# Kernel tuning notes

Measured on AMD Instinct MI355X. Metric: run time of the kernel, lower is better.

## Reference

```python
import jax, jax.numpy as jnp
import numpy as np

LAYER_BS = 63
N_SITES = 12
B = 2048


def _kaiming_uniform(key, shape, fan_in):
    # torch kaiming_uniform_ with a=0: bound = sqrt(6/fan_in)
    bound = np.sqrt(6.0 / fan_in)
    return jax.random.uniform(key, shape, jnp.float32, -bound, bound)


def _cnn12(x, w):
    # x: (B, L, 12, Cin); w: (L, 3*Cin, Cout)
    nn0 = jnp.roll(x, -1, axis=-2) + jnp.roll(x, 3, axis=-2)
    nnn0 = jnp.roll(x, -2, axis=-2) + jnp.roll(x, 4, axis=-2)
    c0 = jnp.concatenate([nn0, nnn0], axis=-1)          # (B,L,12,2*Cin)
    c1 = c0 + jnp.roll(c0, -2, axis=-2)
    allc = jnp.concatenate([x, c1], axis=-1)            # (B,L,12,3*Cin)
    return jnp.einsum('blsc,lco->blso', allc, w)


def _batch_linear(x, w, b):
    # x: (B, L, F); w: (L, F, O); b: (L, O)
    return jnp.einsum('blf,lfo->blo', x, w) + b


def setup_inputs() -> dict:
    key = jax.random.key(0)
    ks = jax.random.split(key, 9)
    zs = jax.random.normal(ks[0], (B, LAYER_BS, N_SITES, 2), jnp.float32)
    # CNN weights: (L, 3*Cin, Cout); kaiming fan_in = 3*Cin
    w1 = _kaiming_uniform(ks[1], (LAYER_BS, 6, 32), 6)
    w2 = _kaiming_uniform(ks[2], (LAYER_BS, 96, 64), 96)
    fw1 = _kaiming_uniform(ks[3], (LAYER_BS, 128, 64), 128)
    fb1 = jax.random.uniform(ks[4], (LAYER_BS, 64), jnp.float32, -1 / np.sqrt(128), 1 / np.sqrt(128))
    fw2 = _kaiming_uniform(ks[5], (LAYER_BS, 64, 64), 64)
    fb2 = jax.random.uniform(ks[6], (LAYER_BS, 64), jnp.float32, -1 / np.sqrt(64), 1 / np.sqrt(64))
    fw3 = _kaiming_uniform(ks[7], (LAYER_BS, 64, 1), 64)
    fb3 = jax.random.uniform(ks[8], (LAYER_BS, 1), jnp.float32, -1 / np.sqrt(64), 1 / np.sqrt(64))
    return {"zs": zs, "w1": w1, "w2": w2, "fw1": fw1, "fb1": fb1,
            "fw2": fw2, "fb2": fb2, "fw3": fw3, "fb3": fb3}


def reference(zs, w1, w2, fw1, fb1, fw2, fb2, fw3, fb3):
    h = jax.nn.relu(_cnn12(zs, w1))                     # (B,L,12,32)
    h = jax.nn.relu(_cnn12(h, w2))                      # (B,L,12,64)
    h = jnp.concatenate([h.mean(axis=-2), h.max(axis=-2)], axis=-1)
    h = jax.nn.relu(_batch_linear(h, fw1, fb1))
    h = jax.nn.relu(_batch_linear(h, fw2, fb2))
    out = _batch_linear(h, fw3, fb3)                    # (B,L,1)
    return out[..., 0]                                  # (B,L)
```

## Files before the change

kernel.cpp:

```cpp
#include <hip/hip_runtime.h>


#define LNUM 63
#define BT 16
#define NBT 128
#define WSL 29184

typedef __attribute__((ext_vector_type(8))) _Float16 half8;
typedef __attribute__((ext_vector_type(2))) _Float16 half2v;
typedef __attribute__((ext_vector_type(4))) float floatx4;
typedef __attribute__((ext_vector_type(4))) unsigned uint4v;

static __device__ __forceinline__ unsigned cvtpk(float a, float b) {
    return __builtin_bit_cast(unsigned, __builtin_amdgcn_cvt_pkrtz(a, b));
}
static __device__ __forceinline__ half2v u2h(unsigned u) { return __builtin_bit_cast(half2v, u); }
static __device__ __forceinline__ float hlo16(unsigned short s) {
    return (float)__builtin_bit_cast(_Float16, s);
}
static __device__ __forceinline__ int w12(int v) { return v >= 12 ? v - 12 : v; }

#define O_POOLDW 3072
#define O_POOLUS 6144
#define O_POOL2  0
#define O_G2     1280

__global__ void prep(const float* __restrict__ w2, const float* __restrict__ fw1,
                     const float* __restrict__ fw2, const float* __restrict__ w1,
                     unsigned short* __restrict__ ws) {
    __shared__ float S[8192];
    const int l = blockIdx.x, r = blockIdx.y, t = threadIdx.x;
    if (r == 0) {
        const float4* src = (const float4*)(w2 + (size_t)l * 6144);
        #pragma unroll
        for (int j = 0; j < 6; ++j) *(float4*)(S + 4 * (t + 256 * j)) = src[t + 256 * j];
        __syncthreads();
        unsigned* dst = (unsigned*)(ws + (size_t)l * WSL);
        #pragma unroll
        for (int j = 0; j < 13; ++j) {
            int i = j * 256 + t, o = i / 52, cp = i - 52 * o, c = 2 * cp;
            dst[i] = cvtpk(S[c * 64 + o], S[c * 64 + 64 + o]);
        }
    } else if (r == 1) {
        const float4* src = (const float4*)(fw1 + (size_t)l * 8192);
        #pragma unroll
        for (int j = 0; j < 8; ++j) *(float4*)(S + 4 * (t + 256 * j)) = src[t + 256 * j];
        __syncthreads();
        unsigned* dst = (unsigned*)(ws + (size_t)l * WSL + 6656);
        #pragma unroll
        for (int j = 0; j < 17; ++j) {
            int i = j * 256 + t, o = i / 68, cp = i - 68 * o;
            dst[i] = cvtpk(S[cp * 64 + o], S[(64 + cp) * 64 + o]);
        }
    } else if (r == 2) {
        const float4* src = (const float4*)(fw2 + (size_t)l * 4096);
        #pragma unroll
        for (int j = 0; j < 4; ++j) *(float4*)(S + 4 * (t + 256 * j)) = src[t + 256 * j];
        __syncthreads();
        unsigned* dst = (unsigned*)(ws + (size_t)l * WSL + 15360);
        #pragma unroll
        for (int j = 0; j < 9; ++j) {
            int i = j * 256 + t, o = i / 36, cp = i - 36 * o, c = 2 * cp;
            dst[i] = cvtpk(S[c * 64 + o], S[c * 64 + 64 + o]);
        }
    } else {
        if (t < 192) S[t] = w1[(size_t)l * 192 + t];
        __syncthreads();
        unsigned* dst = (unsigned*)(ws + (size_t)l * WSL + 19968);
        #pragma unroll
        for (int j = 0; j < 18; ++j) {
            int i = j * 256 + t;
            int row = i / 12, kp = i - 12 * row;
            int s = row >> 5, o = row & 31;
            int d = kp - s; if (d < 0) d += 12;
            unsigned v = 0;
            if (d == 0)                                    v = cvtpk(S[o],       S[32 + o]);
            else if (d == 1 || d == 3 || d == 9 || d == 11) v = cvtpk(S[64 + o],  S[96 + o]);
            else if (d == 2 || d == 4 || d == 8 || d == 10) v = cvtpk(S[128 + o], S[160 + o]);
            dst[i] = v;
        }
    }
}

__global__ __launch_bounds__(256, 4) void fused_nn(
    const float* __restrict__ zs,  const float* __restrict__ w1,
    const float* __restrict__ fb1, const float* __restrict__ fb2,
    const float* __restrict__ fw3, const float* __restrict__ fb3,
    const unsigned short* __restrict__ ws,
    float* __restrict__ out)
{
    __shared__ __align__(16) unsigned U[4160];
    unsigned short* USH = (unsigned short*)U;

    const int t    = threadIdx.x;
    const int lane = t & 63;
    const int wv   = t >> 6;
    const int n    = lane & 15;
    const int quad = lane >> 4;
    const int l    = blockIdx.x / NBT;
    const int b0   = (blockIdx.x % NBT) * BT;

    float4 x0 = {0.f, 0.f, 0.f, 0.f}, x1 = {0.f, 0.f, 0.f, 0.f};
    if (quad < 3) {
        const float* xr = zs + ((size_t)(b0 + n) * LNUM + l) * 24 + quad * 8;
        x0 = *(const float4*)(xr);
        x1 = *(const float4*)(xr + 4);
    }
    uint4v au[6];
    {
        const uint4v* wbt = (const uint4v*)(ws + (size_t)l * WSL + 19968);
        #pragma unroll
        for (int i = 0; i < 6; ++i) {
            const int rt = 6 * wv + i;
            au[i] = (quad < 3) ? wbt[(rt * 16 + n) * 3 + quad] : (uint4v){0u, 0u, 0u, 0u};
        }
    }
    uint4v bwp[3][4];
    {
        const uint4v* w2q = (const uint4v*)(ws + (size_t)l * WSL);
        #pragma unroll
        for (int ks = 0; ks < 3; ++ks)
            #pragma unroll
            for (int nt = 0; nt < 4; ++nt)
                bwp[ks][nt] = w2q[(nt * 16 + n) * 13 + ks * 4 + quad];
    }

    half8 xb;
    {
        uint4v z = {0u, 0u, 0u, 0u};
        if (quad < 3) {
            z.x = cvtpk(x0.x, x0.y); z.y = cvtpk(x0.z, x0.w);
            z.z = cvtpk(x1.x, x1.y); z.w = cvtpk(x1.z, x1.w);
        }
        xb = __builtin_bit_cast(half8, z);
    }
    {
        #pragma unroll
        for (int i = 0; i < 6; ++i) {
            const int rt = 6 * wv + i;
            floatx4 c = __builtin_amdgcn_mfma_f32_16x16x32_f16(
                __builtin_bit_cast(half8, au[i]), xb, (floatx4){0.f, 0.f, 0.f, 0.f}, 0, 0, 0);
            unsigned pk0 = cvtpk(fmaxf(c[0], 0.f), fmaxf(c[1], 0.f));
            unsigned pk1 = cvtpk(fmaxf(c[2], 0.f), fmaxf(c[3], 0.f));
            const int s = rt >> 1;
            const int chunk = (rt & 1) * 2 + (quad >> 1);
            const int dwoff = ((chunk ^ (n & 3)) << 2) | ((quad & 1) << 1);
            *(uint2*)(U + (n * 12 + s) * 20 + dwoff) = make_uint2(pk0, pk1);
        }
    }
    const float bias1 = fb1[(size_t)l * 64 + wv * 16 + n];
    const float bias2 = fb2[(size_t)l * 64 + wv * 16 + n];
    __syncthreads();

    floatx4 acc[3][4];
    #pragma unroll
    for (int mi = 0; mi < 3; ++mi)
        #pragma unroll
        for (int nt = 0; nt < 4; ++nt) acc[mi][nt] = (floatx4){0.f, 0.f, 0.f, 0.f};
    {
        int rb_[3], si_[3], qx_[3];
        #pragma unroll
        for (int mi = 0; mi < 3; ++mi) {
            int row = 48 * wv + 16 * mi + n;
            int bi = row / 12;
            si_[mi] = row - 12 * bi;
            rb_[mi] = bi * 12;
            qx_[mi] = (quad ^ (bi & 3)) << 2;
        }
        const int dA[4] = {1, 11, 3, 9};
        const int dB[4] = {2, 10, 4, 8};
        #pragma unroll
        for (int ks = 0; ks < 3; ++ks) {
            half8 af[3];
            #pragma unroll
            for (int mi = 0; mi < 3; ++mi) {
                const int rb = rb_[mi], s = si_[mi], q4 = qx_[mi];
                if (ks == 0) {
                    af[mi] = *(const half8*)(U + (rb + s) * 20 + q4);
                } else {
                    const int* d = (ks == 1) ? dA : dB;
                    half8 l0 = *(const half8*)(U + (rb + w12(s + d[0])) * 20 + q4);
                    half8 l1 = *(const half8*)(U + (rb + w12(s + d[1])) * 20 + q4);
                    half8 l2 = *(const half8*)(U + (rb + w12(s + d[2])) * 20 + q4);
                    half8 l3 = *(const half8*)(U + (rb + w12(s + d[3])) * 20 + q4);
                    af[mi] = (l0 + l1) + (l2 + l3);
                }
            }
            #pragma unroll
            for (int mi = 0; mi < 3; ++mi)
                #pragma unroll
                for (int nt = 0; nt < 4; ++nt)
                    acc[mi][nt] = __builtin_amdgcn_mfma_f32_16x16x32_f16(
                        af[mi], __builtin_bit_cast(half8, bwp[ks][nt]), acc[mi][nt], 0, 0, 0);
        }
    }
    __syncthreads();

    #pragma unroll
    for (int mi = 0; mi < 3; ++mi) {
        const int rr = 48 * wv + 16 * mi + 4 * quad;
        const int bq = rr / 12;
        const int chk = (rr - 12 * bq) >> 2;
        #pragma unroll
        for (int nt = 0; nt < 4; ++nt) {
            const int ch = nt * 16 + n;
            float r0 = fmaxf(acc[mi][nt][0], 0.f), r1 = fmaxf(acc[mi][nt][1], 0.f);
            float r2 = fmaxf(acc[mi][nt][2], 0.f), r3 = fmaxf(acc[mi][nt][3], 0.f);
            float sm = (r0 + r1) + (r2 + r3);
            float mx = fmaxf(fmaxf(r0, r1), fmaxf(r2, r3));
            U[(bq * 64 + ch) * 3 + chk] = cvtpk(sm, mx);
        }
    }
    __builtin_amdgcn_wave_barrier();

    {
        const unsigned* p = U + t * 12;
        uint4v q0 = *(const uint4v*)(p);
        uint4v q1 = *(const uint4v*)(p + 4);
        uint4v q2 = *(const uint4v*)(p + 8);
        unsigned arr[12] = {q0.x, q0.y, q0.z, q0.w, q1.x, q1.y, q1.z, q1.w,
                            q2.x, q2.y, q2.z, q2.w};
        const int b = t >> 4, ch0 = (t * 4) & 63;
        const _Float16 inv12 = (_Float16)(1.0f / 12.0f);
        unsigned pk[4];
        #pragma unroll
        for (int j = 0; j < 4; ++j) {
            half2v d0 = u2h(arr[3 * j]), d1 = u2h(arr[3 * j + 1]), d2 = u2h(arr[3 * j + 2]);
            _Float16 s = (d0[0] + d1[0]) + d2[0];
            _Float16 m0 = d0[1] > d1[1] ? d0[1] : d1[1];
            _Float16 m  = m0 > d2[1] ? m0 : d2[1];
            half2v pm;
            pm[0] = s * inv12;
            pm[1] = m;
            pk[j] = __builtin_bit_cast(unsigned, pm);
        }
        uint2 w01 = make_uint2(pk[0], pk[1]), w23 = make_uint2(pk[2], pk[3]);
        *(uint2*)(U + O_POOLDW + b * 68 + ch0)     = w01;
        *(uint2*)(U + O_POOLDW + b * 68 + ch0 + 2) = w23;
    }
    __syncthreads();

    {
        const int o = wv * 16 + n;
        floatx4 a1 = (floatx4){bias1, bias1, bias1, bias1};
        const uint4v* f1q = (const uint4v*)(ws + (size_t)l * WSL + 6656);
        #pragma unroll
        for (int ks = 0; ks < 4; ++ks) {
            half8 av = *(const half8*)(USH + O_POOLUS + n * 136 + ks * 32 + quad * 8);
            uint4v bw = f1q[o * 17 + ks * 4 + quad];
            a1 = __builtin_amdgcn_mfma_f32_16x16x32_f16(av, __builtin_bit_cast(half8, bw), a1, 0, 0, 0);
        }
        #pragma unroll
        for (int i = 0; i < 2; ++i) {
            unsigned pk = cvtpk(fmaxf(a1[2 * i], 0.f), fmaxf(a1[2 * i + 1], 0.f));
            USH[O_POOL2 + (quad * 4 + 2 * i)     * 72 + o] = (unsigned short)(pk & 0xffffu);
            USH[O_POOL2 + (quad * 4 + 2 * i + 1) * 72 + o] = (unsigned short)(pk >> 16);
        }
    }
    __syncthreads();

    {
        const int o = wv * 16 + n;
        floatx4 a2 = (floatx4){bias2, bias2, bias2, bias2};
        const uint4v* f2q = (const uint4v*)(ws + (size_t)l * WSL + 15360);
        #pragma unroll
        for (int ks = 0; ks < 2; ++ks) {
            half8 av = *(const half8*)(USH + O_POOL2 + n * 72 + ks * 32 + quad * 8);
            uint4v bw = f2q[o * 9 + ks * 4 + quad];
            a2 = __builtin_amdgcn_mfma_f32_16x16x32_f16(av, __builtin_bit_cast(half8, bw), a2, 0, 0, 0);
        }
        #pragma unroll
        for (int i = 0; i < 2; ++i) {
            unsigned pk = cvtpk(fmaxf(a2[2 * i], 0.f), fmaxf(a2[2 * i + 1], 0.f));
            USH[O_G2 + (quad * 4 + 2 * i)     * 72 + o] = (unsigned short)(pk & 0xffffu);
            USH[O_G2 + (quad * 4 + 2 * i + 1) * 72 + o] = (unsigned short)(pk >> 16);
        }
    }
    __syncthreads();

    if (t < 16) {
        float a = fb3[l];
        const float* w3 = fw3 + (size_t)l * 64;
        #pragma unroll
        for (int c4 = 0; c4 < 16; ++c4) {
            uint2 u2 = *(const uint2*)(USH + O_G2 + t * 72 + c4 * 4);
            float4 w = *(const float4*)(w3 + c4 * 4);
            a += hlo16((unsigned short)(u2.x & 0xffff)) * w.x
               + hlo16((unsigned short)(u2.x >> 16))    * w.y
               + hlo16((unsigned short)(u2.y & 0xffff)) * w.z
               + hlo16((unsigned short)(u2.y >> 16))    * w.w;
        }
        out[(size_t)(b0 + t) * LNUM + l] = a;
    }
}

extern "C" void kernel_launch(void* const* d_in, const int* in_sizes, int n_in,
                              void* d_out, int out_size, void* d_ws, size_t ws_size,
                              hipStream_t stream) {
    const float* zs  = (const float*)d_in[0];
    const float* w1  = (const float*)d_in[1];
    const float* w2  = (const float*)d_in[2];
    const float* fw1 = (const float*)d_in[3];
    const float* fb1 = (const float*)d_in[4];
    const float* fw2 = (const float*)d_in[5];
    const float* fb2 = (const float*)d_in[6];
    const float* fw3 = (const float*)d_in[7];
    const float* fb3 = (const float*)d_in[8];
    float* out = (float*)d_out;
    unsigned short* ws = (unsigned short*)d_ws;

    hipLaunchKernelGGL(prep, dim3(LNUM, 4), dim3(256), 0, stream, w2, fw1, fw2, w1, ws);
    hipLaunchKernelGGL(fused_nn, dim3(LNUM * NBT), dim3(256), 0, stream,
                       zs, w1, fb1, fb2, fw3, fb3, ws, out);
}
```

Baseline: 137.3 us.

## Make layer-1 per-wave over own batch rows and drop block barriers

Layer-1 work is re-partitioned so each wave computes all 24 row tiles for its own four batch elements. Only lanes n<4 write their results, which makes the first shared-memory exchange wave-local, so the two __syncthreads become wave barriers. The weight loads for the three tile groups and the layer-2 B fragments are interleaved with the MFMAs to hide global latency. The swizzle on the intermediate buffer is removed, and a separate partial-pool region doubles LDS use, which may lower occupancy. Each wave now issues four times more layer-1 MFMAs, three quarters of them redundant.

Result: slower. 154.5 us (+12.5%).

```diff
diff --git a/kernel.cpp b/kernel.cpp
--- a/kernel.cpp
+++ b/kernel.cpp
@@ -20,10 +20,11 @@
 }
 static __device__ __forceinline__ int w12(int v) { return v >= 12 ? v - 12 : v; }
 
-#define O_POOLDW 3072
-#define O_POOLUS 6144
+#define O_PART   3840
+#define O_POOLDW 6912
+#define O_POOLUS 13824
 #define O_POOL2  0
-#define O_G2     1280
+#define O_G2     2560
 
 __global__ void prep(const float* __restrict__ w2, const float* __restrict__ fw1,
                      const float* __restrict__ fw2, const float* __restrict__ w1,
@@ -89,7 +90,7 @@
     const unsigned short* __restrict__ ws,
     float* __restrict__ out)
 {
-    __shared__ __align__(16) unsigned U[4160];
+    __shared__ __align__(16) unsigned U[8000];
     unsigned short* USH = (unsigned short*)U;
 
     const int t    = threadIdx.x;
@@ -102,28 +103,21 @@
 
     float4 x0 = {0.f, 0.f, 0.f, 0.f}, x1 = {0.f, 0.f, 0.f, 0.f};
     if (quad < 3) {
-        const float* xr = zs + ((size_t)(b0 + n) * LNUM + l) * 24 + quad * 8;
+        const int gb = b0 + 4 * wv + (n & 3);
+        const float* xr = zs + ((size_t)gb * LNUM + l) * 24 + quad * 8;
         x0 = *(const float4*)(xr);
         x1 = *(const float4*)(xr + 4);
     }
-    uint4v au[6];
-    {
-        const uint4v* wbt = (const uint4v*)(ws + (size_t)l * WSL + 19968);
-        #pragma unroll
-        for (int i = 0; i < 6; ++i) {
-            const int rt = 6 * wv + i;
-            au[i] = (quad < 3) ? wbt[(rt * 16 + n) * 3 + quad] : (uint4v){0u, 0u, 0u, 0u};
-        }
-    }
-    uint4v bwp[3][4];
-    {
-        const uint4v* w2q = (const uint4v*)(ws + (size_t)l * WSL);
-        #pragma unroll
-        for (int ks = 0; ks < 3; ++ks)
-            #pragma unroll
-            for (int nt = 0; nt < 4; ++nt)
-                bwp[ks][nt] = w2q[(nt * 16 + n) * 13 + ks * 4 + quad];
-    }
+    const uint4v* wbt = (const uint4v*)(ws + (size_t)l * WSL + 19968);
+    const uint4v* w2q = (const uint4v*)(ws + (size_t)l * WSL);
+
+    uint4v au0[8], au1[8], au2[8];
+    #pragma unroll
+    for (int i = 0; i < 8; ++i)
+        au0[i] = (quad < 3) ? wbt[((i) * 16 + n) * 3 + quad] : (uint4v){0u, 0u, 0u, 0u};
+    #pragma unroll
+    for (int i = 0; i < 8; ++i)
+        au1[i] = (quad < 3) ? wbt[((8 + i) * 16 + n) * 3 + quad] : (uint4v){0u, 0u, 0u, 0u};
 
     half8 xb;
     {
@@ -134,23 +128,42 @@
         }
         xb = __builtin_bit_cast(half8, z);
     }
-    {
-        #pragma unroll
-        for (int i = 0; i < 6; ++i) {
-            const int rt = 6 * wv + i;
-            floatx4 c = __builtin_amdgcn_mfma_f32_16x16x32_f16(
-                __builtin_bit_cast(half8, au[i]), xb, (floatx4){0.f, 0.f, 0.f, 0.f}, 0, 0, 0);
-            unsigned pk0 = cvtpk(fmaxf(c[0], 0.f), fmaxf(c[1], 0.f));
-            unsigned pk1 = cvtpk(fmaxf(c[2], 0.f), fmaxf(c[3], 0.f));
-            const int s = rt >> 1;
-            const int chunk = (rt & 1) * 2 + (quad >> 1);
-            const int dwoff = ((chunk ^ (n & 3)) << 2) | ((quad & 1) << 1);
-            *(uint2*)(U + (n * 12 + s) * 20 + dwoff) = make_uint2(pk0, pk1);
-        }
-    }
+
+    #define L1_TILE(rt, AU)                                                           \
+    {                                                                                 \
+        floatx4 c = __builtin_amdgcn_mfma_f32_16x16x32_f16(                           \
+            __builtin_bit_cast(half8, AU), xb, (floatx4){0.f, 0.f, 0.f, 0.f}, 0, 0, 0);\
+        unsigned pk0 = cvtpk(fmaxf(c[0], 0.f), fmaxf(c[1], 0.f));                     \
+        unsigned pk1 = cvtpk(fmaxf(c[2], 0.f), fmaxf(c[3], 0.f));                     \
+        if (n < 4) {                                                                  \
+            const int s_ = (rt) >> 1;                                                 \
+            *(uint2*)(U + ((4 * wv + n) * 12 + s_) * 20 + ((rt) & 1) * 8 + 2 * quad)  \
+                = make_uint2(pk0, pk1);                                               \
+        }                                                                             \
+    }
+    {
+        #pragma unroll
+        for (int i = 0; i < 8; ++i) L1_TILE(i, au0[i])
+        #pragma unroll
+        for (int i = 0; i < 8; ++i)
+            au2[i] = (quad < 3) ? wbt[((16 + i) * 16 + n) * 3 + quad] : (uint4v){0u, 0u, 0u, 0u};
+        #pragma unroll
+        for (int i = 0; i < 8; ++i) L1_TILE(8 + i, au1[i])
+    }
+    uint4v bwp[3][4];
+    #pragma unroll
+    for (int ks = 0; ks < 3; ++ks)
+        #pragma unroll
+        for (int nt = 0; nt < 4; ++nt)
+            bwp[ks][nt] = w2q[(nt * 16 + n) * 13 + ks * 4 + quad];
+    {
+        #pragma unroll
+        for (int i = 0; i < 8; ++i) L1_TILE(16 + i, au2[i])
+    }
+    #undef L1_TILE
     const float bias1 = fb1[(size_t)l * 64 + wv * 16 + n];
     const float bias2 = fb2[(size_t)l * 64 + wv * 16 + n];
-    __syncthreads();
+    __builtin_amdgcn_wave_barrier();
 
     floatx4 acc[3][4];
     #pragma unroll
@@ -158,15 +171,15 @@
         #pragma unroll
         for (int nt = 0; nt < 4; ++nt) acc[mi][nt] = (floatx4){0.f, 0.f, 0.f, 0.f};
     {
-        int rb_[3], si_[3], qx_[3];
+        int rb_[3], si_[3];
         #pragma unroll
         for (int mi = 0; mi < 3; ++mi) {
             int row = 48 * wv + 16 * mi + n;
             int bi = row / 12;
             si_[mi] = row - 12 * bi;
             rb_[mi] = bi * 12;
-            qx_[mi] = (quad ^ (bi & 3)) << 2;
-        }
+        }
+        const int q4 = quad * 4;
         const int dA[4] = {1, 11, 3, 9};
         const int dB[4] = {2, 10, 4, 8};
         #pragma unroll
@@ -174,7 +187,7 @@
             half8 af[3];
             #pragma unroll
             for (int mi = 0; mi < 3; ++mi) {
-                const int rb = rb_[mi], s = si_[mi], q4 = qx_[mi];
+                const int rb = rb_[mi], s = si_[mi];
                 if (ks == 0) {
                     af[mi] = *(const half8*)(U + (rb + s) * 20 + q4);
                 } else {
@@ -194,7 +207,7 @@
                         af[mi], __builtin_bit_cast(half8, bwp[ks][nt]), acc[mi][nt], 0, 0, 0);
         }
     }
-    __syncthreads();
+    __builtin_amdgcn_wave_barrier();
 
     #pragma unroll
     for (int mi = 0; mi < 3; ++mi) {
@@ -208,13 +221,13 @@
             float r2 = fmaxf(acc[mi][nt][2], 0.f), r3 = fmaxf(acc[mi][nt][3], 0.f);
             float sm = (r0 + r1) + (r2 + r3);
             float mx = fmaxf(fmaxf(r0, r1), fmaxf(r2, r3));
-            U[(bq * 64 + ch) * 3 + chk] = cvtpk(sm, mx);
+            U[O_PART + (bq * 64 + ch) * 3 + chk] = cvtpk(sm, mx);
         }
     }
     __builtin_amdgcn_wave_barrier();
 
     {
-        const unsigned* p = U + t * 12;
+        const unsigned* p = U + O_PART + t * 12;
         uint4v q0 = *(const uint4v*)(p);
         uint4v q1 = *(const uint4v*)(p + 4);
         uint4v q2 = *(const uint4v*)(p + 8);
```

## Reorder conv1 output to site-major layout so each wave owns sites for pooling

Applied to the files above, without the earlier changes.

Stores the first conv activations site-major (site, batch) rather than batch-major, so each wave's MFMA row tiles cover 3 whole sites across 16 batch entries. Shift lookups become simple site-offset loads without per-row div/mod or XOR swizzle. Pooling is split into per-wave partial sums and maxes over three sites in registers, written to a new LDS region and combined across the four waves after one barrier. This drops a barrier and the 12-way per-thread reduction, but more than doubles LDS use, which may reduce occupancy and may add bank conflicts from the unswizzled layout.

Result: slower. 144.8 us (+5.4%).

```diff
diff --git a/kernel.cpp b/kernel.cpp
--- a/kernel.cpp
+++ b/kernel.cpp
@@ -20,10 +20,11 @@
 }
 static __device__ __forceinline__ int w12(int v) { return v >= 12 ? v - 12 : v; }
 
-#define O_POOLDW 3072
-#define O_POOLUS 6144
+#define O_PART   3840
+#define O_POOLDW 8192
+#define O_POOLUS 16384
 #define O_POOL2  0
-#define O_G2     1280
+#define O_G2     2560
 
 __global__ void prep(const float* __restrict__ w2, const float* __restrict__ fw1,
                      const float* __restrict__ fw2, const float* __restrict__ w1,
@@ -89,7 +90,7 @@
     const unsigned short* __restrict__ ws,
     float* __restrict__ out)
 {
-    __shared__ __align__(16) unsigned U[4160];
+    __shared__ __align__(16) unsigned U[9280];
     unsigned short* USH = (unsigned short*)U;
 
     const int t    = threadIdx.x;
@@ -143,9 +144,7 @@
             unsigned pk0 = cvtpk(fmaxf(c[0], 0.f), fmaxf(c[1], 0.f));
             unsigned pk1 = cvtpk(fmaxf(c[2], 0.f), fmaxf(c[3], 0.f));
             const int s = rt >> 1;
-            const int chunk = (rt & 1) * 2 + (quad >> 1);
-            const int dwoff = ((chunk ^ (n & 3)) << 2) | ((quad & 1) << 1);
-            *(uint2*)(U + (n * 12 + s) * 20 + dwoff) = make_uint2(pk0, pk1);
+            *(uint2*)(U + (s * 16 + n) * 20 + (rt & 1) * 8 + 2 * quad) = make_uint2(pk0, pk1);
         }
     }
     const float bias1 = fb1[(size_t)l * 64 + wv * 16 + n];
@@ -158,15 +157,7 @@
         #pragma unroll
         for (int nt = 0; nt < 4; ++nt) acc[mi][nt] = (floatx4){0.f, 0.f, 0.f, 0.f};
     {
-        int rb_[3], si_[3], qx_[3];
-        #pragma unroll
-        for (int mi = 0; mi < 3; ++mi) {
-            int row = 48 * wv + 16 * mi + n;
-            int bi = row / 12;
-            si_[mi] = row - 12 * bi;
-            rb_[mi] = bi * 12;
-            qx_[mi] = (quad ^ (bi & 3)) << 2;
-        }
+        const int abase = n * 20 + quad * 4;
         const int dA[4] = {1, 11, 3, 9};
         const int dB[4] = {2, 10, 4, 8};
         #pragma unroll
@@ -174,15 +165,15 @@
             half8 af[3];
             #pragma unroll
             for (int mi = 0; mi < 3; ++mi) {
-                const int rb = rb_[mi], s = si_[mi], q4 = qx_[mi];
+                const int s = 3 * wv + mi;
                 if (ks == 0) {
-                    af[mi] = *(const half8*)(U + (rb + s) * 20 + q4);
+                    af[mi] = *(const half8*)(U + s * 320 + abase);
                 } else {
                     const int* d = (ks == 1) ? dA : dB;
-                    half8 l0 = *(const half8*)(U + (rb + w12(s + d[0])) * 20 + q4);
-                    half8 l1 = *(const half8*)(U + (rb + w12(s + d[1])) * 20 + q4);
-                    half8 l2 = *(const half8*)(U + (rb + w12(s + d[2])) * 20 + q4);
-                    half8 l3 = *(const half8*)(U + (rb + w12(s + d[3])) * 20 + q4);
+                    half8 l0 = *(const half8*)(U + w12(s + d[0]) * 320 + abase);
+                    half8 l1 = *(const half8*)(U + w12(s + d[1]) * 320 + abase);
+                    half8 l2 = *(const half8*)(U + w12(s + d[2]) * 320 + abase);
+                    half8 l3 = *(const half8*)(U + w12(s + d[3]) * 320 + abase);
                     af[mi] = (l0 + l1) + (l2 + l3);
                 }
             }
@@ -194,41 +185,38 @@
                         af[mi], __builtin_bit_cast(half8, bwp[ks][nt]), acc[mi][nt], 0, 0, 0);
         }
     }
-    __syncthreads();
 
     #pragma unroll
-    for (int mi = 0; mi < 3; ++mi) {
-        const int rr = 48 * wv + 16 * mi + 4 * quad;
-        const int bq = rr / 12;
-        const int chk = (rr - 12 * bq) >> 2;
+    for (int i = 0; i < 4; ++i) {
+        const int b = 4 * quad + i;
         #pragma unroll
         for (int nt = 0; nt < 4; ++nt) {
-            const int ch = nt * 16 + n;
-            float r0 = fmaxf(acc[mi][nt][0], 0.f), r1 = fmaxf(acc[mi][nt][1], 0.f);
-            float r2 = fmaxf(acc[mi][nt][2], 0.f), r3 = fmaxf(acc[mi][nt][3], 0.f);
-            float sm = (r0 + r1) + (r2 + r3);
-            float mx = fmaxf(fmaxf(r0, r1), fmaxf(r2, r3));
-            U[(bq * 64 + ch) * 3 + chk] = cvtpk(sm, mx);
-        }
-    }
-    __builtin_amdgcn_wave_barrier();
-
-    {
-        const unsigned* p = U + t * 12;
+            float r0 = fmaxf(acc[0][nt][i], 0.f);
+            float r1 = fmaxf(acc[1][nt][i], 0.f);
+            float r2 = fmaxf(acc[2][nt][i], 0.f);
+            float sm = (r0 + r1) + r2;
+            float mx = fmaxf(fmaxf(r0, r1), r2);
+            U[O_PART + wv * 1088 + b * 68 + nt * 16 + n] = cvtpk(sm, mx);
+        }
+    }
+    __syncthreads();
+
+    {
+        const int b = t >> 4, ch0 = (t & 15) * 4;
+        const unsigned* p = U + O_PART + b * 68 + ch0;
         uint4v q0 = *(const uint4v*)(p);
-        uint4v q1 = *(const uint4v*)(p + 4);
-        uint4v q2 = *(const uint4v*)(p + 8);
-        unsigned arr[12] = {q0.x, q0.y, q0.z, q0.w, q1.x, q1.y, q1.z, q1.w,
-                            q2.x, q2.y, q2.z, q2.w};
-        const int b = t >> 4, ch0 = (t * 4) & 63;
+        uint4v q1 = *(const uint4v*)(p + 1088);
+        uint4v q2 = *(const uint4v*)(p + 2176);
+        uint4v q3 = *(const uint4v*)(p + 3264);
         const _Float16 inv12 = (_Float16)(1.0f / 12.0f);
         unsigned pk[4];
         #pragma unroll
         for (int j = 0; j < 4; ++j) {
-            half2v d0 = u2h(arr[3 * j]), d1 = u2h(arr[3 * j + 1]), d2 = u2h(arr[3 * j + 2]);
-            _Float16 s = (d0[0] + d1[0]) + d2[0];
+            half2v d0 = u2h(q0[j]), d1 = u2h(q1[j]), d2 = u2h(q2[j]), d3 = u2h(q3[j]);
+            _Float16 s = (d0[0] + d1[0]) + (d2[0] + d3[0]);
             _Float16 m0 = d0[1] > d1[1] ? d0[1] : d1[1];
-            _Float16 m  = m0 > d2[1] ? m0 : d2[1];
+            _Float16 m1 = d2[1] > d3[1] ? d2[1] : d3[1];
+            _Float16 m  = m0 > m1 ? m0 : m1;
             half2v pm;
             pm[0] = s * inv12;
             pm[1] = m;
```
